# Kernel tuning notes

Hardware: AMD Instinct MI355X
Metric: run time of the kernel (lower is better)

The kernel has to match this reference:

```python
import jax, jax.numpy as jnp
import numpy as np

N_NODES = 50000
N_EDGES = 640000
D_FEAT = 128
D_HID = 128


def _sage_conv(x, src, dst, W_l, b_l, W_r, num_nodes):
    """PyG SAGEConv (aggr='mean'): out = lin_l(mean_j x_j) + lin_r(x_i).

    W_l/W_r are [out, in] (torch Linear convention); lin_r has no bias.
    """
    msgs = x[src]                                               # [E, d]
    agg = jax.ops.segment_sum(msgs, dst, num_segments=num_nodes)
    cnt = jax.ops.segment_sum(jnp.ones((src.shape[0], 1), x.dtype), dst,
                              num_segments=num_nodes)           # [N, 1]
    mean = agg / jnp.maximum(cnt, 1.0)                          # [N, d]
    return mean @ W_l.T + b_l + x @ W_r.T


def setup_inputs() -> dict:
    key = jax.random.key(0)
    ks = jax.random.split(key, 8)
    x = jax.random.normal(ks[0], (N_NODES, D_FEAT), dtype=jnp.float32)
    edge_index = jax.random.randint(ks[1], (2, N_EDGES), 0, N_NODES, dtype=jnp.int64)
    s1 = 1.0 / np.sqrt(D_FEAT)
    s2 = 1.0 / np.sqrt(D_HID)
    W1_l = jax.random.uniform(ks[2], (D_HID, D_FEAT), jnp.float32, -s1, s1)
    b1_l = jnp.zeros((D_HID,), jnp.float32)
    W1_r = jax.random.uniform(ks[3], (D_HID, D_FEAT), jnp.float32, -s1, s1)
    W2_l = jax.random.uniform(ks[4], (D_HID, D_HID), jnp.float32, -s2, s2)
    b2_l = jnp.zeros((D_HID,), jnp.float32)
    W2_r = jax.random.uniform(ks[5], (D_HID, D_HID), jnp.float32, -s2, s2)
    return {"x": x, "edge_index": edge_index, "W1_l": W1_l, "b1_l": b1_l,
            "W1_r": W1_r, "W2_l": W2_l, "b2_l": b2_l, "W2_r": W2_r}


def reference(x, edge_index, W1_l, b1_l, W1_r, W2_l, b2_l, W2_r):
    src, dst = edge_index[0], edge_index[1]
    n = x.shape[0]
    h = _sage_conv(x, src, dst, W1_l, b1_l, W1_r, n)
    h = jax.nn.relu(h)
    h = _sage_conv(h, src, dst, W2_l, b2_l, W2_r, n)
    return jax.nn.relu(h)
```

## Files before the change

### kernel.cpp

```cpp
#include <hip/hip_runtime.h>
#include <hip/hip_bf16.h>

#define N_NODES 50000
#define N_EDGES 640000
#define D 128
#define SCAN_BLK 25

typedef __bf16 bf16x8 __attribute__((ext_vector_type(8)));
typedef float f32x4 __attribute__((ext_vector_type(4)));

__device__ __forceinline__ ushort f2bf(float f) {
    __hip_bfloat16 h = __float2bfloat16(f);
    return *(ushort*)&h;
}
__device__ __forceinline__ float bflo(uint u) { return __uint_as_float(u << 16); }
__device__ __forceinline__ float bfhi(uint u) { return __uint_as_float(u & 0xffff0000u); }

__global__ __launch_bounds__(256) void prep_kernel(const float* __restrict__ x,
                                                   const float* __restrict__ W1l,
                                                   const float* __restrict__ W1r,
                                                   const float* __restrict__ W2l,
                                                   const float* __restrict__ W2r,
                                                   ushort* __restrict__ xb,
                                                   ushort* __restrict__ Wb1,
                                                   ushort* __restrict__ Wb2,
                                                   int* __restrict__ deg) {
    const int b = blockIdx.x;
    const int tid = threadIdx.x;
    if (b < 3125) {
        int i = b * 256 + tid;
        const float4 u0 = *(const float4*)&x[i * 8];
        const float4 u1 = *(const float4*)&x[i * 8 + 4];
        union { ushort u[8]; uint4 v; } p;
        p.u[0] = f2bf(u0.x); p.u[1] = f2bf(u0.y); p.u[2] = f2bf(u0.z); p.u[3] = f2bf(u0.w);
        p.u[4] = f2bf(u1.x); p.u[5] = f2bf(u1.y); p.u[6] = f2bf(u1.z); p.u[7] = f2bf(u1.w);
        *(uint4*)&xb[i * 8] = p.v;
    } else if (b < 3381) {
        int i = (b - 3125) * 256 + tid;
        if (i < 32768) {
            int n = i >> 8, k = i & 255;
            float v = (k < 128) ? W1l[n * 128 + k] : W1r[n * 128 + (k - 128)];
            Wb1[i] = f2bf(v);
        } else {
            int j = i - 32768;
            int n = j >> 8, k = j & 255;
            float v = (k < 128) ? W2l[n * 128 + k] : W2r[n * 128 + (k - 128)];
            Wb2[j] = f2bf(v);
        }
    } else {
        int i = (b - 3381) * 256 + tid;
        if (i < N_NODES) deg[i] = 0;
    }
}

__global__ __launch_bounds__(256) void hist_kernel(const int* __restrict__ dst,
                                                   int* __restrict__ deg) {
    const int base = blockIdx.x * 1024 + threadIdx.x;
    int d0 = dst[base];
    int d1 = dst[base + 256];
    int d2 = dst[base + 512];
    int d3 = dst[base + 768];
    atomicAdd(&deg[d0], 1);
    atomicAdd(&deg[d1], 1);
    atomicAdd(&deg[d2], 1);
    atomicAdd(&deg[d3], 1);
}

__global__ __launch_bounds__(256) void scan1_kernel(const int* __restrict__ deg,
                                                    int* __restrict__ incl,
                                                    int* __restrict__ blockSum) {
    __shared__ int wsum[4];
    const int t = threadIdx.x;
    const int base = blockIdx.x * 2048 + t * 8;
    int v[8];
    int s = 0;
#pragma unroll
    for (int i = 0; i < 8; ++i) {
        int idx = base + i;
        v[i] = (idx < N_NODES) ? deg[idx] : 0;
        s += v[i];
    }
    const int lane = t & 63;
    const int wid = t >> 6;
    int ps = s;
#pragma unroll
    for (int off = 1; off < 64; off <<= 1) {
        int u = __shfl_up(ps, off, 64);
        if (lane >= off) ps += u;
    }
    if (lane == 63) wsum[wid] = ps;
    __syncthreads();
    int wOff = 0;
    for (int w = 0; w < wid; ++w) wOff += wsum[w];
    int run = wOff + ps - s;
#pragma unroll
    for (int i = 0; i < 8; ++i) {
        run += v[i];
        int idx = base + i;
        if (idx < N_NODES) incl[idx] = run;
    }
    if (t == 255) blockSum[blockIdx.x] = wOff + ps;
}

__global__ __launch_bounds__(256) void scan2_kernel(const int* __restrict__ deg,
                                                    const int* __restrict__ incl,
                                                    const int* __restrict__ blockSum,
                                                    int* __restrict__ row_off,
                                                    int* __restrict__ cursor) {
    const int b = blockIdx.x;
    int off = 0;
    for (int i = 0; i < b; ++i) off += blockSum[i];
    const int t = threadIdx.x;
#pragma unroll
    for (int i = 0; i < 8; ++i) {
        int idx = b * 2048 + i * 256 + t;
        if (idx < N_NODES) {
            int inc = incl[idx] + off;
            row_off[idx + 1] = inc;
            cursor[idx] = inc - deg[idx];
        }
    }
    if (b == 0 && t == 0) row_off[0] = 0;
}

__global__ __launch_bounds__(256) void fill_kernel(const int* __restrict__ src,
                                                   const int* __restrict__ dst,
                                                   int* __restrict__ cursor,
                                                   int* __restrict__ esrc) {
    const int base = blockIdx.x * 1024 + threadIdx.x;
    int d0 = dst[base];
    int d1 = dst[base + 256];
    int d2 = dst[base + 512];
    int d3 = dst[base + 768];
    int s0 = src[base];
    int s1 = src[base + 256];
    int s2 = src[base + 512];
    int s3 = src[base + 768];
    int p0 = atomicAdd(&cursor[d0], 1);
    int p1 = atomicAdd(&cursor[d1], 1);
    int p2 = atomicAdd(&cursor[d2], 1);
    int p3 = atomicAdd(&cursor[d3], 1);
    esrc[p0] = s0;
    esrc[p1] = s1;
    esrc[p2] = s2;
    esrc[p3] = s3;
}

__global__ __launch_bounds__(256) void gather_mean(const int* __restrict__ row_off,
                                                   const int* __restrict__ esrc,
                                                   const ushort* __restrict__ feat,
                                                   ushort* __restrict__ mean) {
    const int node = (blockIdx.x * 256 + threadIdx.x) >> 6;
    const int lane = threadIdx.x & 63;
    if (node >= N_NODES) return;
    const int beg = row_off[node];
    const int end = row_off[node + 1];
    const int g = lane >> 4;
    const int c = lane & 15;
    const char* fb = (const char*)feat;
    float acc[8];
#pragma unroll
    for (int r = 0; r < 8; ++r) acc[r] = 0.0f;

    for (int i = beg; i < end; i += 8) {
        int i0 = i + g;
        int i1 = i + 4 + g;
        uint4 v0 = make_uint4(0u, 0u, 0u, 0u);
        uint4 v1 = make_uint4(0u, 0u, 0u, 0u);
        if (i0 < end) {
            int s = esrc[i0];
            v0 = *(const uint4*)(fb + ((size_t)s << 8) + c * 16);
        }
        if (i1 < end) {
            int s = esrc[i1];
            v1 = *(const uint4*)(fb + ((size_t)s << 8) + c * 16);
        }
        acc[0] += bflo(v0.x) + bflo(v1.x);
        acc[1] += bfhi(v0.x) + bfhi(v1.x);
        acc[2] += bflo(v0.y) + bflo(v1.y);
        acc[3] += bfhi(v0.y) + bfhi(v1.y);
        acc[4] += bflo(v0.z) + bflo(v1.z);
        acc[5] += bfhi(v0.z) + bfhi(v1.z);
        acc[6] += bflo(v0.w) + bflo(v1.w);
        acc[7] += bfhi(v0.w) + bfhi(v1.w);
    }
#pragma unroll
    for (int r = 0; r < 8; ++r) {
        acc[r] += __shfl_xor(acc[r], 16, 64);
        acc[r] += __shfl_xor(acc[r], 32, 64);
    }
    if (g == 0) {
        const int dg = end - beg;
        const float inv = (dg > 0) ? 1.0f / (float)dg : 0.0f;
        union { ushort u[8]; uint4 v; } p;
#pragma unroll
        for (int r = 0; r < 8; ++r) p.u[r] = f2bf(acc[r] * inv);
        *(uint4*)((char*)mean + ((size_t)node << 8) + c * 16) = p.v;
    }
}

template <int OUT_BF16>
__global__ __launch_bounds__(256) void sage_mfma(const ushort* __restrict__ feat,
                                                 const ushort* __restrict__ mean,
                                                 const ushort* __restrict__ Wb,
                                                 const float* __restrict__ bias,
                                                 void* __restrict__ outv) {
    __shared__ __align__(16) char As[64 * 512];

    const int tid = threadIdx.x;
    const int nodeBase = blockIdx.x * 64;

    {
        const int row = tid >> 2;
        const int q = tid & 3;
        const int node = nodeBase + row;
        const bool valid = node < N_NODES;
        const ushort* srcp = (q < 2) ? (mean + (size_t)node * D + q * 64)
                                     : (feat + (size_t)node * D + (q - 2) * 64);
        const int swz = (row & 7) << 4;
#pragma unroll
        for (int c = 0; c < 8; ++c) {
            uint4 v = make_uint4(0u, 0u, 0u, 0u);
            if (valid) v = *(const uint4*)(srcp + c * 8);
            int colb = q * 128 + c * 16;
            *(uint4*)(As + row * 512 + (colb ^ swz)) = v;
        }
    }
    __syncthreads();

    const int lane = tid & 63;
    const int w = tid >> 6;
    const int l15 = lane & 15;
    const int lg = lane >> 4;
    const int swz = (l15 & 7) << 4;

    f32x4 acc[4][2];
#pragma unroll
    for (int m = 0; m < 4; ++m) {
        acc[m][0] = (f32x4)(0.0f);
        acc[m][1] = (f32x4)(0.0f);
    }

    const ushort* WA = Wb + (size_t)(w * 32 + l15) * 256 + lg * 8;
    const ushort* WB = WA + 16 * 256;

#pragma unroll
    for (int t = 0; t < 8; ++t) {
        bf16x8 b0 = *(const bf16x8*)(WA + t * 32);
        bf16x8 b1 = *(const bf16x8*)(WB + t * 32);
        const int kb = t * 64 + lg * 16;
#pragma unroll
        for (int m = 0; m < 4; ++m) {
            bf16x8 a = *(const bf16x8*)(As + (m * 16 + l15) * 512 + (kb ^ swz));
            acc[m][0] = __builtin_amdgcn_mfma_f32_16x16x32_bf16(a, b0, acc[m][0], 0, 0, 0);
            acc[m][1] = __builtin_amdgcn_mfma_f32_16x16x32_bf16(a, b1, acc[m][1], 0, 0, 0);
        }
    }

    const int c0 = w * 32 + l15;
    const float bv0 = bias[c0];
    const float bv1 = bias[c0 + 16];
#pragma unroll
    for (int m = 0; m < 4; ++m) {
#pragma unroll
        for (int j = 0; j < 4; ++j) {
            int node = nodeBase + m * 16 + lg * 4 + j;
            if (node < N_NODES) {
                float r0 = fmaxf(acc[m][0][j] + bv0, 0.0f);
                float r1 = fmaxf(acc[m][1][j] + bv1, 0.0f);
                if (OUT_BF16) {
                    ushort* out = (ushort*)outv;
                    out[(size_t)node * D + c0]      = f2bf(r0);
                    out[(size_t)node * D + c0 + 16] = f2bf(r1);
                } else {
                    float* out = (float*)outv;
                    out[(size_t)node * D + c0]      = r0;
                    out[(size_t)node * D + c0 + 16] = r1;
                }
            }
        }
    }
}

extern "C" void kernel_launch(void* const* d_in, const int* in_sizes, int n_in,
                              void* d_out, int out_size, void* d_ws, size_t ws_size,
                              hipStream_t stream) {
    const float* x   = (const float*)d_in[0];
    const int*   ei  = (const int*)d_in[1];
    const int*   src = ei;
    const int*   dst = ei + N_EDGES;
    const float* W1l = (const float*)d_in[2];
    const float* b1  = (const float*)d_in[3];
    const float* W1r = (const float*)d_in[4];
    const float* W2l = (const float*)d_in[5];
    const float* b2  = (const float*)d_in[6];
    const float* W2r = (const float*)d_in[7];
    float* out = (float*)d_out;

    ushort* xb     = (ushort*)d_ws;
    ushort* hb     = xb + (size_t)N_NODES * D;
    ushort* meanb  = hb + (size_t)N_NODES * D;
    int*   row_off = (int*)(meanb + (size_t)N_NODES * D);
    int*   cursor  = row_off + (N_NODES + 1);
    int*   esrc    = cursor + N_NODES;
    int*   deg     = esrc + N_EDGES;
    int*   incl    = deg + N_NODES;
    int*   blockSum= incl + N_NODES;
    ushort* Wb1    = (ushort*)(blockSum + SCAN_BLK);
    ushort* Wb2    = Wb1 + 128 * 256;

    const int edge4Blocks = N_EDGES / 1024;
    const int waveBlocks = (N_NODES * 64 + 255) / 256;
    const int gemmBlocks = (N_NODES + 63) / 64;
    const int prepBlocks = 3125 + 256 + (N_NODES + 255) / 256;

    prep_kernel<<<prepBlocks, 256, 0, stream>>>(x, W1l, W1r, W2l, W2r, xb, Wb1, Wb2, deg);
    hist_kernel<<<edge4Blocks, 256, 0, stream>>>(dst, deg);
    scan1_kernel<<<SCAN_BLK, 256, 0, stream>>>(deg, incl, blockSum);
    scan2_kernel<<<SCAN_BLK, 256, 0, stream>>>(deg, incl, blockSum, row_off, cursor);
    fill_kernel<<<edge4Blocks, 256, 0, stream>>>(src, dst, cursor, esrc);

    gather_mean<<<waveBlocks, 256, 0, stream>>>(row_off, esrc, xb, meanb);
    sage_mfma<1><<<gemmBlocks, 256, 0, stream>>>(xb, meanb, Wb1, b1, hb);

    gather_mean<<<waveBlocks, 256, 0, stream>>>(row_off, esrc, hb, meanb);
    sage_mfma<0><<<gemmBlocks, 256, 0, stream>>>(hb, meanb, Wb2, b2, out);
}
```

Measured before the change: 176.5 us.

## Privatize degree histogram into 8 partitions and fuse histogram into prep kernel

The degree histogram now goes into 8 private copies selected by block index, and the histogram step is folded into the prep kernel, which removes one launch. The scan kernels sum the 8 partitions, and scan2 writes per-partition cursors so that fill_kernel's atomics also hit 8 separate cursor arrays. The aim is to cut atomic contention and save a launch. The costs are a memset of the larger array and 8x more reads in the scan kernels.

```diff
diff --git a/kernel.cpp b/kernel.cpp
--- a/kernel.cpp
+++ b/kernel.cpp
@@ -5,6 +5,7 @@
 #define N_EDGES 640000
 #define D 128
 #define SCAN_BLK 25
+#define PSTRIDE 50048
 
 typedef __bf16 bf16x8 __attribute__((ext_vector_type(8)));
 typedef float f32x4 __attribute__((ext_vector_type(4)));
@@ -21,22 +22,34 @@
                                                    const float* __restrict__ W1r,
                                                    const float* __restrict__ W2l,
                                                    const float* __restrict__ W2r,
+                                                   const int* __restrict__ dst,
                                                    ushort* __restrict__ xb,
                                                    ushort* __restrict__ Wb1,
                                                    ushort* __restrict__ Wb2,
-                                                   int* __restrict__ deg) {
+                                                   int* __restrict__ deg8) {
     const int b = blockIdx.x;
     const int tid = threadIdx.x;
-    if (b < 3125) {
-        int i = b * 256 + tid;
+    if (b < 625) {
+        const int base = b * 1024 + tid;
+        int* dp = deg8 + (b & 7) * PSTRIDE;
+        int d0 = dst[base];
+        int d1 = dst[base + 256];
+        int d2 = dst[base + 512];
+        int d3 = dst[base + 768];
+        atomicAdd(&dp[d0], 1);
+        atomicAdd(&dp[d1], 1);
+        atomicAdd(&dp[d2], 1);
+        atomicAdd(&dp[d3], 1);
+    } else if (b < 3750) {
+        int i = (b - 625) * 256 + tid;
         const float4 u0 = *(const float4*)&x[i * 8];
         const float4 u1 = *(const float4*)&x[i * 8 + 4];
         union { ushort u[8]; uint4 v; } p;
         p.u[0] = f2bf(u0.x); p.u[1] = f2bf(u0.y); p.u[2] = f2bf(u0.z); p.u[3] = f2bf(u0.w);
         p.u[4] = f2bf(u1.x); p.u[5] = f2bf(u1.y); p.u[6] = f2bf(u1.z); p.u[7] = f2bf(u1.w);
         *(uint4*)&xb[i * 8] = p.v;
-    } else if (b < 3381) {
-        int i = (b - 3125) * 256 + tid;
+    } else {
+        int i = (b - 3750) * 256 + tid;
         if (i < 32768) {
             int n = i >> 8, k = i & 255;
             float v = (k < 128) ? W1l[n * 128 + k] : W1r[n * 128 + (k - 128)];
@@ -47,26 +60,10 @@
             float v = (k < 128) ? W2l[n * 128 + k] : W2r[n * 128 + (k - 128)];
             Wb2[j] = f2bf(v);
         }
-    } else {
-        int i = (b - 3381) * 256 + tid;
-        if (i < N_NODES) deg[i] = 0;
-    }
-}
-
-__global__ __launch_bounds__(256) void hist_kernel(const int* __restrict__ dst,
-                                                   int* __restrict__ deg) {
-    const int base = blockIdx.x * 1024 + threadIdx.x;
-    int d0 = dst[base];
-    int d1 = dst[base + 256];
-    int d2 = dst[base + 512];
-    int d3 = dst[base + 768];
-    atomicAdd(&deg[d0], 1);
-    atomicAdd(&deg[d1], 1);
-    atomicAdd(&deg[d2], 1);
-    atomicAdd(&deg[d3], 1);
-}
-
-__global__ __launch_bounds__(256) void scan1_kernel(const int* __restrict__ deg,
+    }
+}
+
+__global__ __launch_bounds__(256) void scan1_kernel(const int* __restrict__ deg8,
                                                     int* __restrict__ incl,
                                                     int* __restrict__ blockSum) {
     __shared__ int wsum[4];
@@ -77,8 +74,13 @@
 #pragma unroll
     for (int i = 0; i < 8; ++i) {
         int idx = base + i;
-        v[i] = (idx < N_NODES) ? deg[idx] : 0;
-        s += v[i];
+        int tot = 0;
+        if (idx < N_NODES) {
+#pragma unroll
+            for (int p = 0; p < 8; ++p) tot += deg8[p * PSTRIDE + idx];
+        }
+        v[i] = tot;
+        s += tot;
     }
     const int lane = t & 63;
     const int wid = t >> 6;
@@ -102,11 +104,11 @@
     if (t == 255) blockSum[blockIdx.x] = wOff + ps;
 }
 
-__global__ __launch_bounds__(256) void scan2_kernel(const int* __restrict__ deg,
+__global__ __launch_bounds__(256) void scan2_kernel(const int* __restrict__ deg8,
                                                     const int* __restrict__ incl,
                                                     const int* __restrict__ blockSum,
                                                     int* __restrict__ row_off,
-                                                    int* __restrict__ cursor) {
+                                                    int* __restrict__ cursor8) {
     const int b = blockIdx.x;
     int off = 0;
     for (int i = 0; i < b; ++i) off += blockSum[i];
@@ -117,7 +119,13 @@
         if (idx < N_NODES) {
             int inc = incl[idx] + off;
             row_off[idx + 1] = inc;
-            cursor[idx] = inc - deg[idx];
+            int dp[8];
+            int dsum = 0;
+#pragma unroll
+            for (int p = 0; p < 8; ++p) { dp[p] = deg8[p * PSTRIDE + idx]; dsum += dp[p]; }
+            int c = inc - dsum;
+#pragma unroll
+            for (int p = 0; p < 8; ++p) { cursor8[p * PSTRIDE + idx] = c; c += dp[p]; }
         }
     }
     if (b == 0 && t == 0) row_off[0] = 0;
@@ -125,9 +133,10 @@
 
 __global__ __launch_bounds__(256) void fill_kernel(const int* __restrict__ src,
                                                    const int* __restrict__ dst,
-                                                   int* __restrict__ cursor,
+                                                   int* __restrict__ cursor8,
                                                    int* __restrict__ esrc) {
     const int base = blockIdx.x * 1024 + threadIdx.x;
+    int* cp = cursor8 + (blockIdx.x & 7) * PSTRIDE;
     int d0 = dst[base];
     int d1 = dst[base + 256];
     int d2 = dst[base + 512];
@@ -136,10 +145,10 @@
     int s1 = src[base + 256];
     int s2 = src[base + 512];
     int s3 = src[base + 768];
-    int p0 = atomicAdd(&cursor[d0], 1);
-    int p1 = atomicAdd(&cursor[d1], 1);
-    int p2 = atomicAdd(&cursor[d2], 1);
-    int p3 = atomicAdd(&cursor[d3], 1);
+    int p0 = atomicAdd(&cp[d0], 1);
+    int p1 = atomicAdd(&cp[d1], 1);
+    int p2 = atomicAdd(&cp[d2], 1);
+    int p3 = atomicAdd(&cp[d3], 1);
     esrc[p0] = s0;
     esrc[p1] = s1;
     esrc[p2] = s2;
@@ -301,10 +310,10 @@
     ushort* hb     = xb + (size_t)N_NODES * D;
     ushort* meanb  = hb + (size_t)N_NODES * D;
     int*   row_off = (int*)(meanb + (size_t)N_NODES * D);
-    int*   cursor  = row_off + (N_NODES + 1);
-    int*   esrc    = cursor + N_NODES;
-    int*   deg     = esrc + N_EDGES;
-    int*   incl    = deg + N_NODES;
+    int*   esrc    = row_off + (N_NODES + 1);
+    int*   deg8    = esrc + N_EDGES;
+    int*   cursor8 = deg8 + 8 * PSTRIDE;
+    int*   incl    = cursor8 + 8 * PSTRIDE;
     int*   blockSum= incl + N_NODES;
     ushort* Wb1    = (ushort*)(blockSum + SCAN_BLK);
     ushort* Wb2    = Wb1 + 128 * 256;
@@ -312,13 +321,14 @@
     const int edge4Blocks = N_EDGES / 1024;
     const int waveBlocks = (N_NODES * 64 + 255) / 256;
     const int gemmBlocks = (N_NODES + 63) / 64;
-    const int prepBlocks = 3125 + 256 + (N_NODES + 255) / 256;
-
-    prep_kernel<<<prepBlocks, 256, 0, stream>>>(x, W1l, W1r, W2l, W2r, xb, Wb1, Wb2, deg);
-    hist_kernel<<<edge4Blocks, 256, 0, stream>>>(dst, deg);
-    scan1_kernel<<<SCAN_BLK, 256, 0, stream>>>(deg, incl, blockSum);
-    scan2_kernel<<<SCAN_BLK, 256, 0, stream>>>(deg, incl, blockSum, row_off, cursor);
-    fill_kernel<<<edge4Blocks, 256, 0, stream>>>(src, dst, cursor, esrc);
+    const int prepBlocks = 625 + 3125 + 256;
+
+    hipMemsetAsync(deg8, 0, sizeof(int) * 8 * PSTRIDE, stream);
+    prep_kernel<<<prepBlocks, 256, 0, stream>>>(x, W1l, W1r, W2l, W2r, dst,
+                                                xb, Wb1, Wb2, deg8);
+    scan1_kernel<<<SCAN_BLK, 256, 0, stream>>>(deg8, incl, blockSum);
+    scan2_kernel<<<SCAN_BLK, 256, 0, stream>>>(deg8, incl, blockSum, row_off, cursor8);
+    fill_kernel<<<edge4Blocks, 256, 0, stream>>>(src, dst, cursor8, esrc);
 
     gather_mean<<<waveBlocks, 256, 0, stream>>>(row_off, esrc, xb, meanb);
     sage_mfma<1><<<gemmBlocks, 256, 0, stream>>>(xb, meanb, Wb1, b1, hb);
```

After: 180.5 us. +2.3%, slower.
